# Kernel tuning notes

Hardware: AMD Instinct MI355X
Metric: run time of the kernel (lower is better)

## Reference

```python
import jax, jax.numpy as jnp
import numpy as np

N_NODES = 100000
N_EDGES = 1600000
IN = 128
HID2 = 128  # hid_size * 2
OUT = 64    # hid_size


def _sage_mean(h, src, dst, W_self, W_neigh, b, n_nodes):
    # DGL SAGEConv('mean'): fc_self(h) + fc_neigh(mean of in-neighbor feats) + bias
    msg = h[src]                                             # [E, d] gather
    msum = jax.ops.segment_sum(msg, dst, num_segments=n_nodes)
    deg = jax.ops.segment_sum(jnp.ones((src.shape[0],), h.dtype), dst,
                              num_segments=n_nodes)
    agg = msum / jnp.clip(deg, 1.0)[:, None]                 # mean, 0 for isolated
    return h @ W_self + agg @ W_neigh + b


def setup_inputs() -> dict:
    key = jax.random.key(0)
    ks = jax.random.split(key, 9)
    s = lambda fan_in: 1.0 / np.sqrt(fan_in)
    return {
        "h": jax.random.normal(ks[0], (N_NODES, IN), jnp.float32),
        "edge_src": jax.random.randint(ks[1], (N_EDGES,), 0, N_NODES, jnp.int32),
        "edge_dst": jax.random.randint(ks[2], (N_EDGES,), 0, N_NODES, jnp.int32),
        "W_self1": jax.random.uniform(ks[3], (IN, HID2), jnp.float32, -s(IN), s(IN)),
        "W_neigh1": jax.random.uniform(ks[4], (IN, HID2), jnp.float32, -s(IN), s(IN)),
        "b1": jnp.zeros((HID2,), jnp.float32),
        "W_self2": jax.random.uniform(ks[5], (HID2, OUT), jnp.float32, -s(HID2), s(HID2)),
        "W_neigh2": jax.random.uniform(ks[6], (HID2, OUT), jnp.float32, -s(HID2), s(HID2)),
        "b2": jnp.zeros((OUT,), jnp.float32),
    }


def reference(h, edge_src, edge_dst, W_self1, W_neigh1, b1, W_self2, W_neigh2, b2):
    n = h.shape[0]
    h1 = jax.nn.relu(_sage_mean(h, edge_src, edge_dst, W_self1, W_neigh1, b1, n))
    h2 = jax.nn.relu(_sage_mean(h1, edge_src, edge_dst, W_self2, W_neigh2, b2, n))
    return h2
```

## Files before the change

kernel.cpp:

```cpp
#include <hip/hip_runtime.h>


typedef __attribute__((ext_vector_type(8))) short short8;
typedef __attribute__((ext_vector_type(4))) float f32x4;
typedef __attribute__((ext_vector_type(2))) float f32x2;

__device__ __forceinline__ ushort f2bf(float f) {
  uint u = __float_as_uint(f);
  u += 0x7fffu + ((u >> 16) & 1u);
  return (ushort)(u >> 16);
}

#define GLDS(src, dst)                                                        \
  __builtin_amdgcn_global_load_lds(                                           \
      (const __attribute__((address_space(1))) void*)(src),                   \
      (__attribute__((address_space(3))) void*)(dst), 16, 0, 0)

#define FENCE() asm volatile("" ::: "memory")
#define LGKM0() asm volatile("s_waitcnt lgkmcnt(0)" ::: "memory")

__global__ __launch_bounds__(256) void k_bhist(const int* __restrict__ dst,
                                               int* __restrict__ bcnt, int E) {
  __shared__ int h[512];
  int t = threadIdx.x;
  for (int i = t; i < 512; i += 256) h[i] = 0;
  __syncthreads();
  int base = blockIdx.x * 4096;
  int end = min(base + 4096, E);
  for (int e = base + t; e < end; e += 256)
    atomicAdd(&h[((uint)dst[e]) >> 8], 1);
  __syncthreads();
  for (int i = t; i < 512; i += 256)
    if (h[i]) atomicAdd(&bcnt[i], h[i]);
}

__global__ __launch_bounds__(512) void k_bscan(const int* __restrict__ bcnt,
                                               int* __restrict__ bbase,
                                               int* __restrict__ bcur, int P, int E) {
  __shared__ int s[512];
  int t = threadIdx.x;
  int v = (t < P) ? bcnt[t] : 0;
  s[t] = v;
  __syncthreads();
  for (int off = 1; off < 512; off <<= 1) {
    int x = (t >= off) ? s[t - off] : 0;
    __syncthreads();
    s[t] += x;
    __syncthreads();
  }
  int ex = s[t] - v;
  if (t < P) {
    bbase[t] = ex;
    bcur[t] = ex;
  }
  if (t == P - 1) bbase[P] = E;
}

__global__ __launch_bounds__(256) void k_bscatter(const int* __restrict__ dst,
                                                  const int* __restrict__ src,
                                                  int* __restrict__ bcur,
                                                  uint* __restrict__ bed, int E, int P) {
  __shared__ int hist[512];
  __shared__ int incl[512];
  __shared__ int gpos[512];
  __shared__ int cur[512];
  __shared__ uint stage[4096];
  __shared__ ushort bof[4096];
  int t = threadIdx.x;
  int base = blockIdx.x * 4096;
  int cnt = min(4096, E - base);
  for (int i = t; i < 512; i += 256) hist[i] = 0;
  __syncthreads();
  for (int i = t; i < cnt; i += 256)
    atomicAdd(&hist[((uint)dst[base + i]) >> 8], 1);
  __syncthreads();
  incl[t] = hist[t];
  incl[t + 256] = hist[t + 256];
  __syncthreads();
  for (int off = 1; off < 512; off <<= 1) {
    int i0 = t, i1 = t + 256;
    int a0 = (i0 >= off) ? incl[i0 - off] : 0;
    int a1 = (i1 >= off) ? incl[i1 - off] : 0;
    __syncthreads();
    incl[i0] += a0;
    incl[i1] += a1;
    __syncthreads();
  }
  cur[t] = incl[t] - hist[t];
  cur[t + 256] = incl[t + 256] - hist[t + 256];
  for (int i = t; i < P; i += 256)
    if (hist[i]) gpos[i] = atomicAdd(&bcur[i], hist[i]);
  __syncthreads();
  for (int i = t; i < cnt; i += 256) {
    int d = dst[base + i];
    int b = ((uint)d) >> 8;
    uint val = (((uint)src[base + i]) << 8) | (uint)(d & 255);
    int slot = atomicAdd(&cur[b], 1);
    stage[slot] = val;
    bof[slot] = (ushort)b;
  }
  __syncthreads();
  for (int i = t; i < cnt; i += 256) {
    int b = bof[i];
    int ex = incl[b] - hist[b];
    bed[gpos[b] + (i - ex)] = stage[i];
  }
}

__global__ __launch_bounds__(256) void k_bcsr(const uint* __restrict__ bed,
                                              const int* __restrict__ bbase,
                                              int* __restrict__ deg,
                                              int* __restrict__ rs,
                                              int* __restrict__ col, int N) {
  __shared__ int dcnt[256];
  __shared__ int sofs[256];
  int b = blockIdx.x, t = threadIdx.x;
  int e0 = bbase[b], e1 = bbase[b + 1];
  dcnt[t] = 0;
  __syncthreads();
  for (int e = e0 + t; e < e1; e += 256) atomicAdd(&dcnt[bed[e] & 255u], 1);
  __syncthreads();
  int v0 = dcnt[t];
  sofs[t] = v0;
  __syncthreads();
  for (int off = 1; off < 256; off <<= 1) {
    int x = (t >= off) ? sofs[t - off] : 0;
    __syncthreads();
    sofs[t] += x;
    __syncthreads();
  }
  int ex = sofs[t] - v0;
  int node = (b << 8) + t;
  if (node < N) {
    deg[node] = v0;
    rs[node] = e0 + ex;
  }
  __syncthreads();
  dcnt[t] = e0 + ex;
  __syncthreads();
  for (int e = e0 + t; e < e1; e += 256) {
    uint v = bed[e];
    int pos = atomicAdd(&dcnt[v & 255u], 1);
    col[pos] = (int)(v >> 8);
  }
}

__global__ __launch_bounds__(256) void k_prep(
    const float* __restrict__ in, const float* __restrict__ Ws1,
    const float* __restrict__ Wn1, const float* __restrict__ Ws2,
    const float* __restrict__ Wn2, ushort* __restrict__ outb,
    uchar* __restrict__ out8, ushort* __restrict__ Wt1,
    ushort* __restrict__ Wt2cat, int n8, int CB) {
  if ((int)blockIdx.x < CB) {
    int i = blockIdx.x * 256 + threadIdx.x;
    if (i >= n8) return;
    const float4* p = reinterpret_cast<const float4*>(in) + i * 2;
    float4 a = p[0], b = p[1];
    ushort u[8];
    u[0] = f2bf(a.x); u[1] = f2bf(a.y); u[2] = f2bf(a.z); u[3] = f2bf(a.w);
    u[4] = f2bf(b.x); u[5] = f2bf(b.y); u[6] = f2bf(b.z); u[7] = f2bf(b.w);
    *reinterpret_cast<ulonglong2*>(outb + (size_t)i * 8) =
        *reinterpret_cast<ulonglong2*>(u);
    uint2 q;
    int w0 = __builtin_amdgcn_cvt_pk_fp8_f32(a.x, a.y, 0, false);
    w0 = __builtin_amdgcn_cvt_pk_fp8_f32(a.z, a.w, w0, true);
    int w1 = __builtin_amdgcn_cvt_pk_fp8_f32(b.x, b.y, 0, false);
    w1 = __builtin_amdgcn_cvt_pk_fp8_f32(b.z, b.w, w1, true);
    q.x = (uint)w0;
    q.y = (uint)w1;
    *reinterpret_cast<uint2*>(out8 + (size_t)i * 8) = q;
  } else {
    int idx = ((int)blockIdx.x - CB) * 256 + threadIdx.x;
    if (idx < 128 * 256) {
      int n = idx >> 8, k = idx & 255;
      float v = (k < 128) ? Ws1[(size_t)k * 128 + n]
                          : Wn1[(size_t)(k - 128) * 128 + n];
      Wt1[idx] = f2bf(v);
    } else if (idx < 128 * 256 + 128 * 128) {
      int j = idx - 128 * 256;
      int n = j >> 7, k = j & 127;
      float v = (n < 64) ? Wn2[(size_t)k * 64 + n] : Ws2[(size_t)k * 64 + (n - 64)];
      Wt2cat[j] = f2bf(v);
    }
  }
}

#define ACC16(v)                                                               \
  do {                                                                         \
    f32x2 f;                                                                   \
    f = __builtin_amdgcn_cvt_pk_f32_fp8((int)(v).x, false); a[0] += f.x; a[1] += f.y;  \
    f = __builtin_amdgcn_cvt_pk_f32_fp8((int)(v).x, true);  a[2] += f.x; a[3] += f.y;  \
    f = __builtin_amdgcn_cvt_pk_f32_fp8((int)(v).y, false); a[4] += f.x; a[5] += f.y;  \
    f = __builtin_amdgcn_cvt_pk_f32_fp8((int)(v).y, true);  a[6] += f.x; a[7] += f.y;  \
    f = __builtin_amdgcn_cvt_pk_f32_fp8((int)(v).z, false); a[8] += f.x; a[9] += f.y;  \
    f = __builtin_amdgcn_cvt_pk_f32_fp8((int)(v).z, true);  a[10] += f.x; a[11] += f.y;\
    f = __builtin_amdgcn_cvt_pk_f32_fp8((int)(v).w, false); a[12] += f.x; a[13] += f.y;\
    f = __builtin_amdgcn_cvt_pk_f32_fp8((int)(v).w, true);  a[14] += f.x; a[15] += f.y;\
  } while (0)

__global__ __launch_bounds__(256) void k_agg1(const uchar* __restrict__ X8,
                                              const int* __restrict__ col,
                                              const int* __restrict__ rs,
                                              const int* __restrict__ deg,
                                              ushort* __restrict__ outb, int n) {
  int node = blockIdx.x * 32 + (threadIdx.x >> 3);
  if (node >= n) return;
  int sl = threadIdx.x & 7;
  int gbase = (threadIdx.x & 63) & ~7;
  int r0 = rs[node], d = deg[node];
  float a[16] = {};
  int j = 0;
  int myc = (sl < min(d, 8)) ? col[r0 + sl] : 0;
  while (j < d) {
    int cnt = min(d - j, 8);
    int nj = j + cnt;
    int ncnt = min(d - nj, 8);
    int c0 = __shfl(myc, gbase + 0, 64);
    int c1 = __shfl(myc, gbase + 1, 64);
    int c2 = __shfl(myc, gbase + 2, 64);
    int c3 = __shfl(myc, gbase + 3, 64);
    int c4 = __shfl(myc, gbase + 4, 64);
    int c5 = __shfl(myc, gbase + 5, 64);
    int c6 = __shfl(myc, gbase + 6, 64);
    int c7 = __shfl(myc, gbase + 7, 64);
    int nmyc = (sl < ncnt) ? col[r0 + nj + sl] : 0;
    uint4 v0, v1, v2, v3, v4, v5, v6, v7;
    if (cnt > 0) v0 = *reinterpret_cast<const uint4*>(X8 + (size_t)c0 * 128 + sl * 16);
    if (cnt > 1) v1 = *reinterpret_cast<const uint4*>(X8 + (size_t)c1 * 128 + sl * 16);
    if (cnt > 2) v2 = *reinterpret_cast<const uint4*>(X8 + (size_t)c2 * 128 + sl * 16);
    if (cnt > 3) v3 = *reinterpret_cast<const uint4*>(X8 + (size_t)c3 * 128 + sl * 16);
    if (cnt > 4) v4 = *reinterpret_cast<const uint4*>(X8 + (size_t)c4 * 128 + sl * 16);
    if (cnt > 5) v5 = *reinterpret_cast<const uint4*>(X8 + (size_t)c5 * 128 + sl * 16);
    if (cnt > 6) v6 = *reinterpret_cast<const uint4*>(X8 + (size_t)c6 * 128 + sl * 16);
    if (cnt > 7) v7 = *reinterpret_cast<const uint4*>(X8 + (size_t)c7 * 128 + sl * 16);
    if (cnt > 0) ACC16(v0);
    if (cnt > 1) ACC16(v1);
    if (cnt > 2) ACC16(v2);
    if (cnt > 3) ACC16(v3);
    if (cnt > 4) ACC16(v4);
    if (cnt > 5) ACC16(v5);
    if (cnt > 6) ACC16(v6);
    if (cnt > 7) ACC16(v7);
    myc = nmyc;
    j = nj;
  }
  float rinv = 1.0f / fmaxf((float)d, 1.0f);
  ushort o[16];
#pragma unroll
  for (int k = 0; k < 16; k++) o[k] = f2bf(a[k] * rinv);
  ulonglong2* dst = reinterpret_cast<ulonglong2*>(outb + (size_t)node * 128 + sl * 16);
  dst[0] = reinterpret_cast<ulonglong2*>(o)[0];
  dst[1] = reinterpret_cast<ulonglong2*>(o)[1];
}

__global__ __launch_bounds__(256) void k_agg_out(const uchar* __restrict__ P8,
                                                 const float* __restrict__ S,
                                                 const int* __restrict__ col,
                                                 const int* __restrict__ rs,
                                                 const int* __restrict__ deg,
                                                 float* __restrict__ out, int n) {
  int node = blockIdx.x * 64 + (threadIdx.x >> 2);
  if (node >= n) return;
  int sl = threadIdx.x & 3;
  int gbase = (threadIdx.x & 63) & ~3;
  int r0 = rs[node], d = deg[node];
  float a[16] = {};
  int j = 0;
  int myc0 = (sl < min(d, 8)) ? col[r0 + sl] : 0;
  int myc1 = (sl + 4 < min(d, 8)) ? col[r0 + 4 + sl] : 0;
  while (j < d) {
    int cnt = min(d - j, 8);
    int nj = j + cnt;
    int ncnt = min(d - nj, 8);
    int c0 = __shfl(myc0, gbase + 0, 64);
    int c1 = __shfl(myc0, gbase + 1, 64);
    int c2 = __shfl(myc0, gbase + 2, 64);
    int c3 = __shfl(myc0, gbase + 3, 64);
    int c4 = __shfl(myc1, gbase + 0, 64);
    int c5 = __shfl(myc1, gbase + 1, 64);
    int c6 = __shfl(myc1, gbase + 2, 64);
    int c7 = __shfl(myc1, gbase + 3, 64);
    int nmyc0 = (sl < ncnt) ? col[r0 + nj + sl] : 0;
    int nmyc1 = (sl + 4 < ncnt) ? col[r0 + nj + 4 + sl] : 0;
    uint4 v0, v1, v2, v3, v4, v5, v6, v7;
    if (cnt > 0) v0 = *reinterpret_cast<const uint4*>(P8 + (size_t)c0 * 64 + sl * 16);
    if (cnt > 1) v1 = *reinterpret_cast<const uint4*>(P8 + (size_t)c1 * 64 + sl * 16);
    if (cnt > 2) v2 = *reinterpret_cast<const uint4*>(P8 + (size_t)c2 * 64 + sl * 16);
    if (cnt > 3) v3 = *reinterpret_cast<const uint4*>(P8 + (size_t)c3 * 64 + sl * 16);
    if (cnt > 4) v4 = *reinterpret_cast<const uint4*>(P8 + (size_t)c4 * 64 + sl * 16);
    if (cnt > 5) v5 = *reinterpret_cast<const uint4*>(P8 + (size_t)c5 * 64 + sl * 16);
    if (cnt > 6) v6 = *reinterpret_cast<const uint4*>(P8 + (size_t)c6 * 64 + sl * 16);
    if (cnt > 7) v7 = *reinterpret_cast<const uint4*>(P8 + (size_t)c7 * 64 + sl * 16);
    if (cnt > 0) ACC16(v0);
    if (cnt > 1) ACC16(v1);
    if (cnt > 2) ACC16(v2);
    if (cnt > 3) ACC16(v3);
    if (cnt > 4) ACC16(v4);
    if (cnt > 5) ACC16(v5);
    if (cnt > 6) ACC16(v6);
    if (cnt > 7) ACC16(v7);
    myc0 = nmyc0;
    myc1 = nmyc1;
    j = nj;
  }
  float rinv = 1.0f / fmaxf((float)d, 1.0f);
  const float4* sp = reinterpret_cast<const float4*>(S + (size_t)node * 64 + sl * 16);
  float4* op = reinterpret_cast<float4*>(out + (size_t)node * 64 + sl * 16);
#pragma unroll
  for (int q = 0; q < 4; q++) {
    float4 s = sp[q];
    float4 o;
    o.x = fmaxf(a[q * 4 + 0] * rinv + s.x, 0.f);
    o.y = fmaxf(a[q * 4 + 1] * rinv + s.y, 0.f);
    o.z = fmaxf(a[q * 4 + 2] * rinv + s.z, 0.f);
    o.w = fmaxf(a[q * 4 + 3] * rinv + s.w, 0.f);
    op[q] = o;
  }
}

__global__ __launch_bounds__(512) void k_persist(const ushort* __restrict__ Xb,
                                                 const ushort* __restrict__ Gb,
                                                 const ushort* __restrict__ Wt1,
                                                 const ushort* __restrict__ Wt2,
                                                 const float* __restrict__ b1,
                                                 const float* __restrict__ b2,
                                                 uchar* __restrict__ P8,
                                                 float* __restrict__ S2,
                                                 int M, int ntiles) {
  __shared__ ushort W1s[128 * 256];
  __shared__ ushort W2s[128 * 128];
  __shared__ char Xs[64 * 256 * 2];

  const int t = threadIdx.x;
  const int lane = t & 63;
  const int w = t >> 6;
  const int wm = w >> 2, wn = w & 3;

#pragma unroll
  for (int i = 0; i < 8; i++) {
    int g = t + 512 * i;
    int row = g >> 5, kph = g & 31;
    const ushort* src = Wt1 + (size_t)row * 256 + ((kph ^ (row & 7)) << 3);
    char* dst = (char*)W1s + ((g & ~63) << 4);
    GLDS(src, dst);
  }
#pragma unroll
  for (int i = 0; i < 4; i++) {
    int g = t + 512 * i;
    int row = g >> 4, kph = g & 15;
    const ushort* src = Wt2 + (size_t)row * 128 + ((kph ^ (row & 7)) << 3);
    char* dst = (char*)W2s + ((g & ~63) << 4);
    GLDS(src, dst);
  }

  float bb1[2], bb2[2];
#pragma unroll
  for (int fn = 0; fn < 2; fn++) {
    int colg = wn * 32 + fn * 16 + (lane & 15);
    bb1[fn] = b1[colg];
    bb2[fn] = (colg >= 64) ? b2[colg - 64] : 0.f;
  }

  int tile = blockIdx.x;
  if (tile >= ntiles) return;

  uint4 xr0, xr1, xr2, xr3;
#define LOADX(tl)                                                              \
  {                                                                            \
    int g, row, kk, gm;                                                        \
    const ushort* s;                                                           \
    g = t;            row = g >> 5; kk = (g & 31) ^ (row & 7);                 \
    gm = min((tl) * 64 + row, M - 1);                                          \
    s = (kk < 16) ? Xb + (size_t)gm * 128 + kk * 8                             \
                  : Gb + (size_t)gm * 128 + (kk - 16) * 8;                     \
    xr0 = *reinterpret_cast<const uint4*>(s);                                  \
    g = t + 512;      row = g >> 5; kk = (g & 31) ^ (row & 7);                 \
    gm = min((tl) * 64 + row, M - 1);                                          \
    s = (kk < 16) ? Xb + (size_t)gm * 128 + kk * 8                             \
                  : Gb + (size_t)gm * 128 + (kk - 16) * 8;                     \
    xr1 = *reinterpret_cast<const uint4*>(s);                                  \
    g = t + 1024;     row = g >> 5; kk = (g & 31) ^ (row & 7);                 \
    gm = min((tl) * 64 + row, M - 1);                                          \
    s = (kk < 16) ? Xb + (size_t)gm * 128 + kk * 8                             \
                  : Gb + (size_t)gm * 128 + (kk - 16) * 8;                     \
    xr2 = *reinterpret_cast<const uint4*>(s);                                  \
    g = t + 1536;     row = g >> 5; kk = (g & 31) ^ (row & 7);                 \
    gm = min((tl) * 64 + row, M - 1);                                          \
    s = (kk < 16) ? Xb + (size_t)gm * 128 + kk * 8                             \
                  : Gb + (size_t)gm * 128 + (kk - 16) * 8;                     \
    xr3 = *reinterpret_cast<const uint4*>(s);                                  \
  }
#define WRITEX()                                                               \
  {                                                                            \
    *reinterpret_cast<uint4*>(Xs + (size_t)t * 16) = xr0;                      \
    *reinterpret_cast<uint4*>(Xs + (size_t)(t + 512) * 16) = xr1;              \
    *reinterpret_cast<uint4*>(Xs + (size_t)(t + 1024) * 16) = xr2;             \
    *reinterpret_cast<uint4*>(Xs + (size_t)(t + 1536) * 16) = xr3;             \
  }

  LOADX(tile);
  WRITEX();
  __syncthreads();

  while (true) {
    int next = tile + gridDim.x;
    bool more = (next < ntiles);
    if (more) LOADX(next);

    f32x4 acc[2][2] = {};
#pragma unroll
    for (int ks = 0; ks < 8; ks++) {
      int ga = ks * 4 + (lane >> 4);
      short8 af[2], bf[2];
#pragma unroll
      for (int fm = 0; fm < 2; fm++) {
        int row = wm * 32 + fm * 16 + (lane & 15);
        af[fm] = *reinterpret_cast<const short8*>(
            Xs + row * 512 + ((ga ^ (row & 7)) << 4));
      }
#pragma unroll
      for (int fn = 0; fn < 2; fn++) {
        int colr = wn * 32 + fn * 16 + (lane & 15);
        bf[fn] = *reinterpret_cast<const short8*>(
            (char*)W1s + colr * 512 + ((ga ^ (colr & 7)) << 4));
      }
#pragma unroll
      for (int fm = 0; fm < 2; fm++)
#pragma unroll
        for (int fn = 0; fn < 2; fn++)
          acc[fm][fn] = __builtin_amdgcn_mfma_f32_16x16x32_bf16(
              af[fm], bf[fn], acc[fm][fn], 0, 0, 0);
    }

    __builtin_amdgcn_s_barrier();
    FENCE();

#pragma unroll
    for (int fn = 0; fn < 2; fn++) {
      int colg = wn * 32 + fn * 16 + (lane & 15);
      int gg = colg >> 3, cb = (colg & 7) * 2;
#pragma unroll
      for (int fm = 0; fm < 2; fm++) {
#pragma unroll
        for (int r = 0; r < 4; r++) {
          int rowl = wm * 32 + fm * 16 + (lane >> 4) * 4 + r;
          ushort hv = f2bf(fmaxf(acc[fm][fn][r] + bb1[fn], 0.f));
          *reinterpret_cast<ushort*>(
              Xs + rowl * 256 + ((gg ^ (rowl & 7)) << 4) + cb) = hv;
        }
      }
    }
    LGKM0();
    __builtin_amdgcn_s_barrier();
    FENCE();

    f32x4 acc2[2][2] = {};
#pragma unroll
    for (int ks = 0; ks < 4; ks++) {
      int gk = ks * 4 + (lane >> 4);
      short8 af[2], bf[2];
#pragma unroll
      for (int fm = 0; fm < 2; fm++) {
        int row = wm * 32 + fm * 16 + (lane & 15);
        af[fm] = *reinterpret_cast<const short8*>(
            Xs + row * 256 + ((gk ^ (row & 7)) << 4));
      }
#pragma unroll
      for (int fn = 0; fn < 2; fn++) {
        int colr = wn * 32 + fn * 16 + (lane & 15);
        bf[fn] = *reinterpret_cast<const short8*>(
            (char*)W2s + colr * 256 + ((gk ^ (colr & 7)) << 4));
      }
#pragma unroll
      for (int fm = 0; fm < 2; fm++)
#pragma unroll
        for (int fn = 0; fn < 2; fn++)
          acc2[fm][fn] = __builtin_amdgcn_mfma_f32_16x16x32_bf16(
              af[fm], bf[fn], acc2[fm][fn], 0, 0, 0);
    }

#pragma unroll
    for (int fn = 0; fn < 2; fn++) {
      int colg = wn * 32 + fn * 16 + (lane & 15);
#pragma unroll
      for (int fm = 0; fm < 2; fm++) {
#pragma unroll
        for (int r = 0; r < 4; r++) {
          int rowg = tile * 64 + wm * 32 + fm * 16 + (lane >> 4) * 4 + r;
          if (rowg >= M) continue;
          if (colg < 64) {
            float v = acc2[fm][fn][r];
            int b8 = __builtin_amdgcn_cvt_pk_fp8_f32(v, v, 0, false);
            P8[(size_t)rowg * 64 + colg] = (uchar)(b8 & 0xff);
          } else {
            S2[(size_t)rowg * 64 + (colg - 64)] = acc2[fm][fn][r] + bb2[fn];
          }
        }
      }
    }

    if (!more) break;
    __builtin_amdgcn_s_barrier();
    FENCE();
    WRITEX();
    LGKM0();
    __builtin_amdgcn_s_barrier();
    FENCE();
    tile = next;
  }
#undef LOADX
#undef WRITEX
}

extern "C" void kernel_launch(void* const* d_in, const int* in_sizes, int n_in,
                              void* d_out, int out_size, void* d_ws, size_t ws_size,
                              hipStream_t stream) {
  const float* h = (const float*)d_in[0];
  const int* esrc = (const int*)d_in[1];
  const int* edst = (const int*)d_in[2];
  const float* Ws1 = (const float*)d_in[3];
  const float* Wn1 = (const float*)d_in[4];
  const float* b1 = (const float*)d_in[5];
  const float* Ws2 = (const float*)d_in[6];
  const float* Wn2 = (const float*)d_in[7];
  const float* b2 = (const float*)d_in[8];
  float* out = (float*)d_out;

  const int N = in_sizes[0] / 128;
  const int E = in_sizes[1];
  const int P = (N + 255) >> 8;

  char* base = (char*)d_ws;
  size_t off = 0;
  auto alloc = [&](size_t bytes) {
    size_t o = off;
    off += (bytes + 255) & ~(size_t)255;
    return o;
  };
  int* deg = (int*)(base + alloc((size_t)N * 4));
  int* rs = (int*)(base + alloc((size_t)N * 4));
  int* bcnt = (int*)(base + alloc(513 * 4));
  int* bbase = (int*)(base + alloc(513 * 4));
  int* bcur = (int*)(base + alloc(513 * 4));
  uint* bed = (uint*)(base + alloc((size_t)E * 4));
  int* col = (int*)(base + alloc((size_t)E * 4));
  ushort* hb = (ushort*)(base + alloc((size_t)N * 128 * 2));
  uchar* h8 = (uchar*)(base + alloc((size_t)N * 128));
  ushort* aggb = (ushort*)(base + alloc((size_t)N * 128 * 2));
  ushort* Wt1 = (ushort*)(base + alloc(128 * 256 * 2));
  ushort* Wt2cat = (ushort*)(base + alloc(128 * 128 * 2));
  uchar* p8 = (uchar*)bed;
  float* s2f = (float*)aggb;

  const int NCH = (E + 4095) / 4096;
  const int NT = (N + 63) / 64;
  const int n8 = N * 128 / 8;
  const int CB = (n8 + 255) / 256;
  const int WB = (128 * 256 + 128 * 128) / 256;

  (void)hipMemsetAsync(bcnt, 0, 513 * 4, stream);
  k_bhist<<<NCH, 256, 0, stream>>>(edst, bcnt, E);
  k_bscan<<<1, 512, 0, stream>>>(bcnt, bbase, bcur, P, E);
  k_bscatter<<<NCH, 256, 0, stream>>>(edst, esrc, bcur, bed, E, P);
  k_bcsr<<<P, 256, 0, stream>>>(bed, bbase, deg, rs, col, N);

  k_prep<<<CB + WB, 256, 0, stream>>>(h, Ws1, Wn1, Ws2, Wn2, hb, h8, Wt1,
                                      Wt2cat, n8, CB);

  k_agg1<<<(N + 31) / 32, 256, 0, stream>>>(h8, col, rs, deg, aggb, N);
  k_persist<<<256, 512, 0, stream>>>(hb, aggb, Wt1, Wt2cat, b1, b2, p8, s2f, N, NT);
  k_agg_out<<<(N + 63) / 64, 256, 0, stream>>>(p8, s2f, col, rs, deg, out, N);
}
```

Measured before the change: 159.2 us.

## Shrink persistent GEMM tile to 32 rows and hold W2 in registers

```diff
diff --git a/kernel.cpp b/kernel.cpp
--- a/kernel.cpp
+++ b/kernel.cpp
@@ -318,23 +318,19 @@
   }
 }
 
-__global__ __launch_bounds__(512) void k_persist(const ushort* __restrict__ Xb,
-                                                 const ushort* __restrict__ Gb,
-                                                 const ushort* __restrict__ Wt1,
-                                                 const ushort* __restrict__ Wt2,
-                                                 const float* __restrict__ b1,
-                                                 const float* __restrict__ b2,
-                                                 uchar* __restrict__ P8,
-                                                 float* __restrict__ S2,
-                                                 int M, int ntiles) {
+__global__ __launch_bounds__(512, 4) void k_persist(
+    const ushort* __restrict__ Xb, const ushort* __restrict__ Gb,
+    const ushort* __restrict__ Wt1, const ushort* __restrict__ Wt2,
+    const float* __restrict__ b1, const float* __restrict__ b2,
+    uchar* __restrict__ P8, float* __restrict__ S2, int M, int ntiles) {
   __shared__ ushort W1s[128 * 256];
-  __shared__ ushort W2s[128 * 128];
-  __shared__ char Xs[64 * 256 * 2];
+  __shared__ char Xs[32 * 512];
 
   const int t = threadIdx.x;
   const int lane = t & 63;
-  const int w = t >> 6;
-  const int wm = w >> 2, wn = w & 3;
+  const int wn = t >> 6;
+  const int l15 = lane & 15;
+  const int grp = lane >> 4;
 
 #pragma unroll
   for (int i = 0; i < 8; i++) {
@@ -344,58 +340,41 @@
     char* dst = (char*)W1s + ((g & ~63) << 4);
     GLDS(src, dst);
   }
-#pragma unroll
-  for (int i = 0; i < 4; i++) {
-    int g = t + 512 * i;
-    int row = g >> 4, kph = g & 15;
-    const ushort* src = Wt2 + (size_t)row * 128 + ((kph ^ (row & 7)) << 3);
-    char* dst = (char*)W2s + ((g & ~63) << 4);
-    GLDS(src, dst);
-  }
-
-  float bb1[2], bb2[2];
-#pragma unroll
-  for (int fn = 0; fn < 2; fn++) {
-    int colg = wn * 32 + fn * 16 + (lane & 15);
-    bb1[fn] = b1[colg];
-    bb2[fn] = (colg >= 64) ? b2[colg - 64] : 0.f;
-  }
+
+  const int colg = wn * 16 + l15;
+  short8 w2f[4];
+#pragma unroll
+  for (int ks = 0; ks < 4; ks++) {
+    int gk = ks * 4 + grp;
+    w2f[ks] = *reinterpret_cast<const short8*>(Wt2 + (size_t)colg * 128 + gk * 8);
+  }
+
+  const float bb1 = b1[colg];
+  const float bb2 = (colg >= 64) ? b2[colg - 64] : 0.f;
 
   int tile = blockIdx.x;
   if (tile >= ntiles) return;
 
-  uint4 xr0, xr1, xr2, xr3;
+  uint4 xr0, xr1;
 #define LOADX(tl)                                                              \
   {                                                                            \
     int g, row, kk, gm;                                                        \
     const ushort* s;                                                           \
-    g = t;            row = g >> 5; kk = (g & 31) ^ (row & 7);                 \
-    gm = min((tl) * 64 + row, M - 1);                                          \
+    g = t;        row = g >> 5; kk = (g & 31) ^ (row & 7);                     \
+    gm = min((tl) * 32 + row, M - 1);                                          \
     s = (kk < 16) ? Xb + (size_t)gm * 128 + kk * 8                             \
                   : Gb + (size_t)gm * 128 + (kk - 16) * 8;                     \
     xr0 = *reinterpret_cast<const uint4*>(s);                                  \
-    g = t + 512;      row = g >> 5; kk = (g & 31) ^ (row & 7);                 \
-    gm = min((tl) * 64 + row, M - 1);                                          \
+    g = t + 512;  row = g >> 5; kk = (g & 31) ^ (row & 7);                     \
+    gm = min((tl) * 32 + row, M - 1);                                          \
     s = (kk < 16) ? Xb + (size_t)gm * 128 + kk * 8                             \
                   : Gb + (size_t)gm * 128 + (kk - 16) * 8;                     \
     xr1 = *reinterpret_cast<const uint4*>(s);                                  \
-    g = t + 1024;     row = g >> 5; kk = (g & 31) ^ (row & 7);                 \
-    gm = min((tl) * 64 + row, M - 1);                                          \
-    s = (kk < 16) ? Xb + (size_t)gm * 128 + kk * 8                             \
-                  : Gb + (size_t)gm * 128 + (kk - 16) * 8;                     \
-    xr2 = *reinterpret_cast<const uint4*>(s);                                  \
-    g = t + 1536;     row = g >> 5; kk = (g & 31) ^ (row & 7);                 \
-    gm = min((tl) * 64 + row, M - 1);                                          \
-    s = (kk < 16) ? Xb + (size_t)gm * 128 + kk * 8                             \
-                  : Gb + (size_t)gm * 128 + (kk - 16) * 8;                     \
-    xr3 = *reinterpret_cast<const uint4*>(s);                                  \
   }
 #define WRITEX()                                                               \
   {                                                                            \
     *reinterpret_cast<uint4*>(Xs + (size_t)t * 16) = xr0;                      \
     *reinterpret_cast<uint4*>(Xs + (size_t)(t + 512) * 16) = xr1;              \
-    *reinterpret_cast<uint4*>(Xs + (size_t)(t + 1024) * 16) = xr2;             \
-    *reinterpret_cast<uint4*>(Xs + (size_t)(t + 1536) * 16) = xr3;             \
   }
 
   LOADX(tile);
@@ -407,44 +386,36 @@
     bool more = (next < ntiles);
     if (more) LOADX(next);
 
-    f32x4 acc[2][2] = {};
+    f32x4 acc[2] = {};
 #pragma unroll
     for (int ks = 0; ks < 8; ks++) {
-      int ga = ks * 4 + (lane >> 4);
-      short8 af[2], bf[2];
+      int ga = ks * 4 + grp;
+      short8 af[2], bf;
 #pragma unroll
       for (int fm = 0; fm < 2; fm++) {
-        int row = wm * 32 + fm * 16 + (lane & 15);
+        int row = fm * 16 + l15;
         af[fm] = *reinterpret_cast<const short8*>(
             Xs + row * 512 + ((ga ^ (row & 7)) << 4));
       }
-#pragma unroll
-      for (int fn = 0; fn < 2; fn++) {
-        int colr = wn * 32 + fn * 16 + (lane & 15);
-        bf[fn] = *reinterpret_cast<const short8*>(
-            (char*)W1s + colr * 512 + ((ga ^ (colr & 7)) << 4));
-      }
+      bf = *reinterpret_cast<const short8*>(
+          (char*)W1s + colg * 512 + ((ga ^ (colg & 7)) << 4));
 #pragma unroll
       for (int fm = 0; fm < 2; fm++)
-#pragma unroll
-        for (int fn = 0; fn < 2; fn++)
-          acc[fm][fn] = __builtin_amdgcn_mfma_f32_16x16x32_bf16(
-              af[fm], bf[fn], acc[fm][fn], 0, 0, 0);
+        acc[fm] = __builtin_amdgcn_mfma_f32_16x16x32_bf16(af[fm], bf, acc[fm],
+                                                          0, 0, 0);
     }
 
     __builtin_amdgcn_s_barrier();
     FENCE();
 
-#pragma unroll
-    for (int fn = 0; fn < 2; fn++) {
-      int colg = wn * 32 + fn * 16 + (lane & 15);
+    {
       int gg = colg >> 3, cb = (colg & 7) * 2;
 #pragma unroll
       for (int fm = 0; fm < 2; fm++) {
 #pragma unroll
         for (int r = 0; r < 4; r++) {
-          int rowl = wm * 32 + fm * 16 + (lane >> 4) * 4 + r;
-          ushort hv = f2bf(fmaxf(acc[fm][fn][r] + bb1[fn], 0.f));
+          int rowl = fm * 16 + grp * 4 + r;
+          ushort hv = f2bf(fmaxf(acc[fm][r] + bb1, 0.f));
           *reinterpret_cast<ushort*>(
               Xs + rowl * 256 + ((gg ^ (rowl & 7)) << 4) + cb) = hv;
         }
@@ -454,47 +425,32 @@
     __builtin_amdgcn_s_barrier();
     FENCE();
 
-    f32x4 acc2[2][2] = {};
+    f32x4 acc2[2] = {};
 #pragma unroll
     for (int ks = 0; ks < 4; ks++) {
-      int gk = ks * 4 + (lane >> 4);
-      short8 af[2], bf[2];
+      int gk = ks * 4 + grp;
 #pragma unroll
       for (int fm = 0; fm < 2; fm++) {
-        int row = wm * 32 + fm * 16 + (lane & 15);
-        af[fm] = *reinterpret_cast<const short8*>(
+        int row = fm * 16 + l15;
+        short8 af = *reinterpret_cast<const short8*>(
             Xs + row * 256 + ((gk ^ (row & 7)) << 4));
+        acc2[fm] = __builtin_amdgcn_mfma_f32_16x16x32_bf16(af, w2f[ks],
+                                                           acc2[fm], 0, 0, 0);
       }
-#pragma unroll
-      for (int fn = 0; fn < 2; fn++) {
-        int colr = wn * 32 + fn * 16 + (lane & 15);
-        bf[fn] = *reinterpret_cast<const short8*>(
-            (char*)W2s + colr * 256 + ((gk ^ (colr & 7)) << 4));
-      }
-#pragma unroll
-      for (int fm = 0; fm < 2; fm++)
-#pragma unroll
-        for (int fn = 0; fn < 2; fn++)
-          acc2[fm][fn] = __builtin_amdgcn_mfma_f32_16x16x32_bf16(
-              af[fm], bf[fn], acc2[fm][fn], 0, 0, 0);
     }
 
 #pragma unroll
-    for (int fn = 0; fn < 2; fn++) {
-      int colg = wn * 32 + fn * 16 + (lane & 15);
-#pragma unroll
-      for (int fm = 0; fm < 2; fm++) {
-#pragma unroll
-        for (int r = 0; r < 4; r++) {
-          int rowg = tile * 64 + wm * 32 + fm * 16 + (lane >> 4) * 4 + r;
-          if (rowg >= M) continue;
-          if (colg < 64) {
-            float v = acc2[fm][fn][r];
-            int b8 = __builtin_amdgcn_cvt_pk_fp8_f32(v, v, 0, false);
-            P8[(size_t)rowg * 64 + colg] = (uchar)(b8 & 0xff);
-          } else {
-            S2[(size_t)rowg * 64 + (colg - 64)] = acc2[fm][fn][r] + bb2[fn];
-          }
+    for (int fm = 0; fm < 2; fm++) {
+#pragma unroll
+      for (int r = 0; r < 4; r++) {
+        int rowg = tile * 32 + fm * 16 + grp * 4 + r;
+        if (rowg >= M) continue;
+        if (colg < 64) {
+          float v = acc2[fm][r];
+          int b8 = __builtin_amdgcn_cvt_pk_fp8_f32(v, v, 0, false);
+          P8[(size_t)rowg * 64 + colg] = (uchar)(b8 & 0xff);
+        } else {
+          S2[(size_t)rowg * 64 + (colg - 64)] = acc2[fm][r] + bb2;
         }
       }
     }
@@ -553,7 +509,7 @@
   float* s2f = (float*)aggb;
 
   const int NCH = (E + 4095) / 4096;
-  const int NT = (N + 63) / 64;
+  const int NT = (N + 31) / 32;
   const int n8 = N * 128 / 8;
   const int CB = (n8 + 255) / 256;
   const int WB = (128 * 256 + 128 * 128) / 256;
@@ -568,6 +524,6 @@
                                       Wt2cat, n8, CB);
 
   k_agg1<<<(N + 31) / 32, 256, 0, stream>>>(h8, col, rs, deg, aggb, N);
-  k_persist<<<256, 512, 0, stream>>>(hb, aggb, Wt1, Wt2cat, b1, b2, p8, s2f, N, NT);
+  k_persist<<<512, 512, 0, stream>>>(hb, aggb, Wt1, Wt2cat, b1, b2, p8, s2f, N, NT);
   k_agg_out<<<(N + 63) / 64, 256, 0, stream>>>(p8, s2f, col, rs, deg, out, N);
 }
```

Measured after the change: 156.2 us. About the same (-1.9%).
